# Kernel optimization log

Measured on AMD Instinct MI355X. Metric: run time of the kernel, lower is better.

Reference implementation:

```python
import jax, jax.numpy as jnp
import numpy as np

H, LMAX, NSEG, EPS = 8, 2, 16, 1e-7
S = (LMAX + 1) ** 2  # 9 spherical components
L_OF_M = jnp.asarray(np.floor(np.sqrt(np.arange(S))).astype(np.int32))  # degree l of each m-component


def so3_linear(x, W, b):
    # x [n,S,Cin]; W [LMAX+1,Cin,Cout] per-degree weights; bias only on l=0 (invariant) component
    y = jnp.einsum('nsi,sio->nso', x, W[L_OF_M])
    return y + b[None, None, :] * (jnp.arange(S) == 0)[None, :, None]


def equiv_layernorm(x, gamma, beta):
    # x [N,S,C]; standard LN on l=0 scalars, RMS-of-irrep-norm scaling (equivariant) for l>0
    x0 = x[:, 0, :]
    mu = jnp.mean(x0, -1, keepdims=True)
    var = jnp.mean((x0 - mu) ** 2, -1, keepdims=True)
    outs = [(((x0 - mu) / jnp.sqrt(var + EPS)) * gamma[0] + beta)[:, None, :]]
    for l in range(1, LMAX + 1):
        xl = x[:, l * l:(l + 1) * (l + 1), :]               # [N,2l+1,C]
        n2 = jnp.mean(xl * xl, axis=1)                      # [N,C] mean sq over m
        rms = jnp.sqrt(jnp.mean(n2, -1, keepdims=True) + EPS)  # [N,1]
        outs.append(xl / rms[:, None, :] * gamma[l][None, None, :])
    return jnp.concatenate(outs, axis=1)


def setup_inputs() -> dict:
    key = jax.random.key(0)
    ks = jax.random.split(key, 12)
    N, E, CIN, CH = 512, 8192, 128, 256
    return dict(
        q=jax.random.normal(ks[0], (N, S, CIN), jnp.float32),
        k=jax.random.normal(ks[1], (N, S, CIN), jnp.float32),
        v=jax.random.normal(ks[2], (N, S, CIN), jnp.float32),
        envelope=jax.random.uniform(ks[3], (E,), jnp.float32),
        attn_bias=jax.random.normal(ks[4], (H, E), jnp.float32),
        atom_index=jax.random.randint(ks[5], (E,), 0, N),
        batch_index=jnp.sort(jax.random.randint(ks[6], (E,), 0, NSEG)),
        edge_map_tab=jax.random.randint(ks[7], (E,), 0, E),
        Wq=jax.random.normal(ks[8], (LMAX + 1, CIN, CH), jnp.float32) / np.float32(np.sqrt(CIN)),
        bq=jnp.zeros((CH,), jnp.float32),
        Wk=jax.random.normal(ks[9], (LMAX + 1, CIN, CH), jnp.float32) / np.float32(np.sqrt(CIN)),
        bk=jnp.zeros((CH,), jnp.float32),
        Wv=jax.random.normal(ks[10], (LMAX + 1, CIN, CH), jnp.float32) / np.float32(np.sqrt(CIN)),
        bv=jnp.zeros((CH,), jnp.float32),
        gamma=jnp.ones((LMAX + 1, CH), jnp.float32),
        beta=jnp.zeros((CH,), jnp.float32),
        Wo=jax.random.normal(ks[11], (LMAX + 1, CH, CIN), jnp.float32) / np.float32(np.sqrt(CH)),
        bo=jnp.zeros((CIN,), jnp.float32),
    )


def reference(q, k, v, envelope, attn_bias, atom_index, batch_index, edge_map_tab,
              Wq, bq, Wk, bk, Wv, bv, gamma, beta, Wo, bo):
    N, E = q.shape[0], atom_index.shape[0]
    qh = so3_linear(q, Wq, bq)                      # [N,S,CH]
    kh = so3_linear(k, Wk, bk)[atom_index]          # [E,S,CH] gather per edge
    vh = so3_linear(v, Wv, bv)[atom_index]
    CH = qh.shape[-1]
    d = CH // H
    qh = qh.reshape(N, S, H, d).transpose(2, 0, 1, 3).reshape(H, N, S * d)
    kh = kh.reshape(E, S, H, d).transpose(2, 0, 1, 3).reshape(H, E, S * d)
    vh = vh.reshape(E, S, H, d).transpose(2, 0, 1, 3).reshape(H, E, S * d)
    scale = np.float32(np.sqrt(d / 3.0) / d)
    scores = jnp.einsum('hnf,hef->hne', qh * scale, kh)         # [H,N,E]
    scores = scores + attn_bias[:, edge_map_tab][:, None, :]
    env_e = envelope[edge_map_tab]                               # [E]
    # smooth scatter softmax grouped by batch_index over edge axis
    st = scores.transpose(2, 0, 1)                               # [E,H,N]
    mx = jax.ops.segment_max(st, batch_index, num_segments=NSEG)
    rec = jnp.exp(st - mx[batch_index]) * env_e[:, None, None]
    den = jax.ops.segment_sum(rec, batch_index, num_segments=NSEG)
    attn = rec / (den[batch_index] + 1e-16)
    attn = (attn * env_e[:, None, None]).transpose(1, 2, 0)      # [H,N,E]
    out = jnp.einsum('hne,hef->hnf', attn, vh)                   # [H,N,S*d]
    out = out.transpose(1, 0, 2).reshape(N, H, S, d).transpose(0, 2, 1, 3).reshape(N, S, CH)
    out = equiv_layernorm(out, gamma, beta)
    return so3_linear(out, Wo, bo)
```

## Files before the change

kernel.cpp:

```cpp
#include <hip/hip_runtime.h>
#include <hip/hip_bf16.h>
#include <math.h>

#define NH 8
#define SDIM 9
#define NSEG 16
#define NATOM 512
#define NEDGE 8192
#define CIN 128
#define CHN 256
#define DH 32
#define FDIM 288
#define EPS 1e-7f
#define SCALE 0.10206207261596577f

typedef __attribute__((ext_vector_type(8))) short bf16x8;
typedef __attribute__((ext_vector_type(8))) short short8;
typedef __attribute__((ext_vector_type(4))) float f32x4;

__device__ inline float blockReduceMax(float v, float* red) {
    #pragma unroll
    for (int off = 32; off; off >>= 1) v = fmaxf(v, __shfl_xor(v, off, 64));
    int lane = threadIdx.x & 63, wid = threadIdx.x >> 6;
    if (lane == 0) red[wid] = v;
    __syncthreads();
    v = fmaxf(fmaxf(red[0], red[1]), fmaxf(red[2], red[3]));
    __syncthreads();
    return v;
}
__device__ inline int lower_bound_batch(const int* __restrict__ b, int val) {
    int lo = 0, hi = NEDGE;
    while (lo < hi) {
        int mid = (lo + hi) >> 1;
        if (b[mid] < val) lo = mid + 1; else hi = mid;
    }
    return lo;
}
__device__ inline ushort f2bu(float x) {
    __hip_bfloat16 b = __float2bfloat16(x);
    return *(ushort*)&b;
}

__global__ void __launch_bounds__(256) wtrans(const float* __restrict__ Wq, const float* __restrict__ Wk,
                                              const float* __restrict__ Wv, const float* __restrict__ Wo,
                                              ushort* __restrict__ WqT, ushort* __restrict__ WkT,
                                              ushort* __restrict__ WvT, ushort* __restrict__ WoT) {
    const int bid = blockIdx.x;
    const int tid = threadIdx.x;
    __shared__ float tile[64][33];
    const float* src; ushort* dst; int R, C, r0, c0;
    if (bid < 144) {
        const int z = bid / 48;
        const int rem = bid % 48;
        const int l = rem >> 4;
        const int t = rem & 15;
        R = CIN; C = CHN;
        r0 = (t >> 3) * 64; c0 = (t & 7) * 32;
        src = ((z == 0) ? Wq : (z == 1) ? Wk : Wv) + (size_t)l * R * C;
        dst = ((z == 0) ? WqT : (z == 1) ? WkT : WvT) + (size_t)l * R * C;
    } else {
        const int rem = bid - 144;
        const int l = rem >> 4;
        const int t = rem & 15;
        R = CHN; C = CIN;
        r0 = (t >> 2) * 64; c0 = (t & 3) * 32;
        src = Wo + (size_t)l * R * C;
        dst = WoT + (size_t)l * R * C;
    }
    #pragma unroll
    for (int p = 0; p < 8; ++p) {
        int row = p * 8 + (tid >> 5);
        int col = tid & 31;
        tile[row][col] = src[(size_t)(r0 + row) * C + c0 + col];
    }
    __syncthreads();
    #pragma unroll
    for (int p = 0; p < 8; ++p) {
        int c = p * 4 + (tid >> 6);
        int rr = tid & 63;
        dst[(size_t)(c0 + c) * R + r0 + rr] = f2bu(tile[rr][c]);
    }
}

__global__ void __launch_bounds__(256) stage1(const int* __restrict__ batch,
                                              const int* __restrict__ am, const int* __restrict__ emap,
                                              const float* __restrict__ envelope,
                                              const float* __restrict__ attn_bias,
                                              float* __restrict__ E1, float* __restrict__ E2,
                                              const float* __restrict__ q, const float* __restrict__ k,
                                              const float* __restrict__ v,
                                              const ushort* __restrict__ WqT, const ushort* __restrict__ WkT,
                                              const ushort* __restrict__ WvT,
                                              const float* __restrict__ bq, const float* __restrict__ bk,
                                              const float* __restrict__ bv,
                                              ushort* __restrict__ qhB,
                                              ushort* __restrict__ khB,
                                              ushort* __restrict__ vhT,
                                              float* __restrict__ stats) {
    const int bid = blockIdx.x;
    const int tid = threadIdx.x;
    if (bid < NSEG * NH) {
        const int seg = bid & (NSEG - 1), h = bid >> 4;
        __shared__ float e1[NATOM];
        __shared__ float e2[NATOM];
        __shared__ float red[4];
        e1[tid] = 0.f; e1[tid + 256] = 0.f;
        e2[tid] = 0.f; e2[tid + 256] = 0.f;
        const float* bh = attn_bias + (size_t)h * NEDGE;
        float mv = -1e30f;
        for (int e = tid; e < NEDGE; e += 256) mv = fmaxf(mv, bh[e]);
        const float mb = blockReduceMax(mv, red);
        const int st = lower_bound_batch(batch, seg);
        const int en = lower_bound_batch(batch, seg + 1);
        for (int e = st + tid; e < en; e += 256) {
            int m = am[e], em = emap[e];
            float ev = envelope[em];
            float eb = __expf(bh[em] - mb);
            atomicAdd(&e1[m], ev * eb);
            atomicAdd(&e2[m], ev * ev * eb);
        }
        __syncthreads();
        size_t base = ((size_t)h * NSEG + seg) * NATOM;
        E1[base + tid] = e1[tid]; E1[base + tid + 256] = e1[tid + 256];
        E2[base + tid] = e2[tid]; E2[base + tid + 256] = e2[tid + 256];
        return;
    }
    if (bid < NSEG * NH + 432) {
        const int idx = bid - NSEG * NH;
        const int z = idx / 144;
        const int rem = idx - z * 144;
        const int s = rem >> 4;
        const int n0 = (rem & 15) * 32;
        const int l = (s == 0) ? 0 : ((s < 4) ? 1 : 2);
        const float* x = (z == 0) ? q : (z == 1) ? k : v;
        const ushort* WT = ((z == 0) ? WqT : (z == 1) ? WkT : WvT) + (size_t)l * CIN * CHN;
        const float* bias = (z == 0) ? bq : (z == 1) ? bk : bv;
        const int lane = tid & 63, w = tid >> 6;
        const int wr = w >> 1, wc = w & 1;
        const int r = lane & 15, kg = lane >> 4;
        const int arow = n0 + 16 * wr + r;
        const float* xrow = x + ((size_t)arow * SDIM + s) * CIN;
        f32x4 acc[8] = {};
        #pragma unroll
        for (int ks = 0; ks < 4; ++ks) {
            const int k0 = ks * 32 + kg * 8;
            float4 x0 = *(const float4*)(xrow + k0);
            float4 x1 = *(const float4*)(xrow + k0 + 4);
            bf16x8 a;
            a[0] = f2bu(x0.x); a[1] = f2bu(x0.y); a[2] = f2bu(x0.z); a[3] = f2bu(x0.w);
            a[4] = f2bu(x1.x); a[5] = f2bu(x1.y); a[6] = f2bu(x1.z); a[7] = f2bu(x1.w);
            #pragma unroll
            for (int j = 0; j < 8; ++j) {
                const int o = 128 * wc + 16 * j + r;
                bf16x8 bf = *(const bf16x8*)(WT + (size_t)o * CIN + k0);
                acc[j] = __builtin_amdgcn_mfma_f32_16x16x32_bf16(a, bf, acc[j], 0, 0, 0);
            }
        }
        const float sc = (z == 0) ? SCALE : 1.0f;
        #pragma unroll
        for (int j = 0; j < 8; ++j) {
            const int o = 128 * wc + 16 * j + r;
            const float bb = (s == 0) ? bias[o] : 0.f;
            const int h = o >> 5, dj = o & 31;
            const int f = s * DH + dj;
            if (z < 2) {
                ushort* dst = (z == 0) ? qhB : khB;
                #pragma unroll
                for (int p = 0; p < 4; ++p) {
                    int row = n0 + 16 * wr + kg * 4 + p;
                    dst[((size_t)h * NATOM + row) * FDIM + f] = f2bu((acc[j][p] + bb) * sc);
                }
            } else {
                ushort* dst = vhT + ((size_t)h * FDIM + f) * NATOM;
                #pragma unroll
                for (int p = 0; p < 4; ++p) {
                    int row = n0 + 16 * wr + kg * 4 + p;
                    dst[row] = f2bu(acc[j][p] + bb);
                }
            }
        }
        return;
    }
    {
        float4 z4 = {0.f, 0.f, 0.f, 0.f};
        float4* sp = (float4*)stats;
        sp[tid] = z4;
        sp[tid + 256] = z4;
    }
}

#define SBST 520
__global__ void __launch_bounds__(512) attn_fused(const ushort* __restrict__ qhB,
                                                  const ushort* __restrict__ khB,
                                                  const float* __restrict__ E1,
                                                  const float* __restrict__ E2,
                                                  ushort* __restrict__ attnB) {
    const int h = blockIdx.y;
    const int n0 = blockIdx.x * 16;
    __shared__ ushort sbuf[16 * SBST];
    __shared__ float rowmax[8][16];
    __shared__ float Dpart[8][16][NSEG];
    __shared__ float invDs[16][NSEG];
    const int tid = threadIdx.x;
    const int lane = tid & 63, w = tid >> 6;
    const int r = lane & 15, kg = lane >> 4;
    const ushort* A = qhB + (size_t)h * NATOM * FDIM;
    const ushort* B = khB + (size_t)h * NATOM * FDIM;
    const float* e1g = E1 + (size_t)h * NSEG * NATOM;
    const float* e2g = E2 + (size_t)h * NSEG * NATOM;
    const int ar = n0 + r;
    f32x4 acc[4] = {};
    #pragma unroll
    for (int ks = 0; ks < FDIM / 32; ++ks) {
        const int k0 = ks * 32 + kg * 8;
        bf16x8 a = *(const bf16x8*)(A + (size_t)ar * FDIM + k0);
        #pragma unroll
        for (int j = 0; j < 4; ++j) {
            const int bcol = w * 64 + 16 * j + r;
            bf16x8 b = *(const bf16x8*)(B + (size_t)bcol * FDIM + k0);
            acc[j] = __builtin_amdgcn_mfma_f32_16x16x32_bf16(a, b, acc[j], 0, 0, 0);
        }
    }
    float pm[4];
    #pragma unroll
    for (int p = 0; p < 4; ++p) {
        float m = fmaxf(fmaxf(acc[0][p], acc[1][p]), fmaxf(acc[2][p], acc[3][p]));
        pm[p] = m;
    }
    #pragma unroll
    for (int mk = 1; mk < 16; mk <<= 1)
        #pragma unroll
        for (int p = 0; p < 4; ++p) pm[p] = fmaxf(pm[p], __shfl_xor(pm[p], mk, 64));
    if (r == 0) {
        #pragma unroll
        for (int p = 0; p < 4; ++p) rowmax[w][kg * 4 + p] = pm[p];
    }
    __syncthreads();
    float mx[4];
    #pragma unroll
    for (int p = 0; p < 4; ++p) {
        const int row = kg * 4 + p;
        float m = rowmax[0][row];
        #pragma unroll
        for (int ww2 = 1; ww2 < 8; ++ww2) m = fmaxf(m, rowmax[ww2][row]);
        mx[p] = m;
    }
    float es[4][4];
    #pragma unroll
    for (int j = 0; j < 4; ++j)
        #pragma unroll
        for (int p = 0; p < 4; ++p) es[j][p] = __expf(acc[j][p] - mx[p]);
    float Dp[4][NSEG] = {};
    #pragma unroll
    for (int j = 0; j < 4; ++j) {
        const int col = w * 64 + 16 * j + r;
        #pragma unroll
        for (int g = 0; g < NSEG; ++g) {
            float e1 = e1g[(size_t)g * NATOM + col];
            #pragma unroll
            for (int p = 0; p < 4; ++p) Dp[p][g] += es[j][p] * e1;
        }
    }
    #pragma unroll
    for (int mk = 1; mk < 16; mk <<= 1)
        #pragma unroll
        for (int p = 0; p < 4; ++p)
            #pragma unroll
            for (int g = 0; g < NSEG; ++g) Dp[p][g] += __shfl_xor(Dp[p][g], mk, 64);
    if (r == 0) {
        #pragma unroll
        for (int p = 0; p < 4; ++p)
            #pragma unroll
            for (int g = 0; g < NSEG; ++g) Dpart[w][kg * 4 + p][g] = Dp[p][g];
    }
    __syncthreads();
    if (tid < 256) {
        const int row = tid >> 4, g = tid & 15;
        float d = 0.f;
        #pragma unroll
        for (int ww2 = 0; ww2 < 8; ++ww2) d += Dpart[ww2][row][g];
        invDs[row][g] = 1.0f / (d + 1e-30f);
    }
    __syncthreads();
    float iv[4][NSEG];
    #pragma unroll
    for (int p = 0; p < 4; ++p)
        #pragma unroll
        for (int g = 0; g < NSEG; ++g) iv[p][g] = invDs[kg * 4 + p][g];
    #pragma unroll
    for (int j = 0; j < 4; ++j) {
        const int col = w * 64 + 16 * j + r;
        float ww[4] = {};
        #pragma unroll
        for (int g = 0; g < NSEG; ++g) {
            float e2 = e2g[(size_t)g * NATOM + col];
            #pragma unroll
            for (int p = 0; p < 4; ++p) ww[p] += e2 * iv[p][g];
        }
        #pragma unroll
        for (int p = 0; p < 4; ++p)
            sbuf[(kg * 4 + p) * SBST + col] = f2bu(es[j][p] * ww[p]);
    }
    __syncthreads();
    {
        ushort* dst = attnB + ((size_t)h * NATOM + n0) * NATOM;
        #pragma unroll
        for (int i = tid * 8; i < 16 * NATOM; i += 4096) {
            const int row = i >> 9, col = i & 511;
            *(short8*)(dst + (size_t)row * NATOM + col) = *(short8*)(sbuf + row * SBST + col);
        }
    }
}

__global__ void __launch_bounds__(256) gemm_out_stats(const ushort* __restrict__ attnB,
                                                      const ushort* __restrict__ vhT,
                                                      float* __restrict__ attnOut,
                                                      float* __restrict__ stats) {
    const int h = blockIdx.z;
    const int fb = blockIdx.x;
    const int n0 = blockIdx.y * 64;
    const int tid = threadIdx.x;
    const int lane = tid & 63, w = tid >> 6;
    const int r = lane & 15, kg = lane >> 4;
    const ushort* A = attnB + (size_t)h * NATOM * NATOM;
    const ushort* B = vhT + (size_t)h * FDIM * NATOM;
    const int ar = n0 + 16 * w + r;
    f32x4 acc[2] = {};
    #pragma unroll 4
    for (int ks = 0; ks < NATOM / 32; ++ks) {
        const int k0 = ks * 32 + kg * 8;
        bf16x8 a = *(const bf16x8*)(A + (size_t)ar * NATOM + k0);
        bf16x8 b0 = *(const bf16x8*)(B + (size_t)(32 * fb + r) * NATOM + k0);
        bf16x8 b1 = *(const bf16x8*)(B + (size_t)(32 * fb + 16 + r) * NATOM + k0);
        acc[0] = __builtin_amdgcn_mfma_f32_16x16x32_bf16(a, b0, acc[0], 0, 0, 0);
        acc[1] = __builtin_amdgcn_mfma_f32_16x16x32_bf16(a, b1, acc[1], 0, 0, 0);
    }
    float sA[4], sB[4];
    #pragma unroll
    for (int p = 0; p < 4; ++p) { sA[p] = 0.f; sB[p] = 0.f; }
    #pragma unroll
    for (int j = 0; j < 2; ++j) {
        const int dj = 16 * j + r;
        #pragma unroll
        for (int p = 0; p < 4; ++p) {
            const int row = n0 + 16 * w + kg * 4 + p;
            float x = acc[j][p];
            attnOut[((size_t)row * SDIM + fb) * CHN + h * DH + dj] = x;
            sA[p] += x;
            sB[p] += x * x;
        }
    }
    #pragma unroll
    for (int mk = 1; mk < 16; mk <<= 1)
        #pragma unroll
        for (int p = 0; p < 4; ++p) {
            sA[p] += __shfl_xor(sA[p], mk, 64);
            sB[p] += __shfl_xor(sB[p], mk, 64);
        }
    if (r == 0) {
        #pragma unroll
        for (int p = 0; p < 4; ++p) {
            const int row = n0 + 16 * w + kg * 4 + p;
            if (fb == 0) {
                atomicAdd(&stats[row * 4 + 0], sA[p]);
                atomicAdd(&stats[row * 4 + 1], sB[p]);
            } else if (fb < 4) {
                atomicAdd(&stats[row * 4 + 2], sB[p]);
            } else {
                atomicAdd(&stats[row * 4 + 3], sB[p]);
            }
        }
    }
}

__global__ void __launch_bounds__(256) so3out_ln(const float* __restrict__ attnOut,
                                                 const float* __restrict__ stats,
                                                 const float* __restrict__ gamma,
                                                 const float* __restrict__ beta,
                                                 const ushort* __restrict__ WoT,
                                                 const float* __restrict__ bo,
                                                 float* __restrict__ out) {
    const int s = blockIdx.y;
    const int n0 = blockIdx.x * 16;
    const int l = (s == 0) ? 0 : ((s < 4) ? 1 : 2);
    const int tid = threadIdx.x;
    const int lane = tid & 63, w = tid >> 6;
    const int r = lane & 15, kg = lane >> 4;
    const int ar = n0 + r;
    float mu, ivl;
    {
        float s0 = stats[ar * 4 + 0];
        float q0 = stats[ar * 4 + 1];
        float q1 = stats[ar * 4 + 2];
        float q2 = stats[ar * 4 + 3];
        float m0 = s0 * (1.0f / CHN);
        float var = q0 * (1.0f / CHN) - m0 * m0;
        if (s == 0) { mu = m0; ivl = 1.0f / sqrtf(var + EPS); }
        else if (s < 4) { mu = 0.f; ivl = 1.0f / sqrtf(q1 * (1.0f / (3 * CHN)) + EPS); }
        else { mu = 0.f; ivl = 1.0f / sqrtf(q2 * (1.0f / (5 * CHN)) + EPS); }
    }
    const float* xrow = attnOut + ((size_t)ar * SDIM + s) * CHN;
    const float* gl = gamma + l * CHN;
    const ushort* B = WoT + (size_t)l * CIN * CHN;
    f32x4 acc[2] = {};
    #pragma unroll
    for (int ks = 0; ks < CHN / 32; ++ks) {
        const int k0 = ks * 32 + kg * 8;
        float4 x0 = *(const float4*)(xrow + k0);
        float4 x1 = *(const float4*)(xrow + k0 + 4);
        float4 g0 = *(const float4*)(gl + k0);
        float4 g1 = *(const float4*)(gl + k0 + 4);
        float y[8];
        y[0] = (x0.x - mu) * ivl * g0.x; y[1] = (x0.y - mu) * ivl * g0.y;
        y[2] = (x0.z - mu) * ivl * g0.z; y[3] = (x0.w - mu) * ivl * g0.w;
        y[4] = (x1.x - mu) * ivl * g1.x; y[5] = (x1.y - mu) * ivl * g1.y;
        y[6] = (x1.z - mu) * ivl * g1.z; y[7] = (x1.w - mu) * ivl * g1.w;
        if (s == 0) {
            float4 b0 = *(const float4*)(beta + k0);
            float4 b1 = *(const float4*)(beta + k0 + 4);
            y[0] += b0.x; y[1] += b0.y; y[2] += b0.z; y[3] += b0.w;
            y[4] += b1.x; y[5] += b1.y; y[6] += b1.z; y[7] += b1.w;
        }
        bf16x8 a;
        #pragma unroll
        for (int jj = 0; jj < 8; ++jj) a[jj] = f2bu(y[jj]);
        bf16x8 b0f = *(const bf16x8*)(B + (size_t)(32 * w + r) * CHN + k0);
        bf16x8 b1f = *(const bf16x8*)(B + (size_t)(32 * w + 16 + r) * CHN + k0);
        acc[0] = __builtin_amdgcn_mfma_f32_16x16x32_bf16(a, b0f, acc[0], 0, 0, 0);
        acc[1] = __builtin_amdgcn_mfma_f32_16x16x32_bf16(a, b1f, acc[1], 0, 0, 0);
    }
    #pragma unroll
    for (int j = 0; j < 2; ++j) {
        const int o = 32 * w + 16 * j + r;
        const float badd = (s == 0) ? bo[o] : 0.f;
        #pragma unroll
        for (int p = 0; p < 4; ++p) {
            const int n = n0 + kg * 4 + p;
            out[((size_t)n * SDIM + s) * CIN + o] = acc[j][p] + badd;
        }
    }
}

extern "C" void kernel_launch(void* const* d_in, const int* in_sizes, int n_in,
                              void* d_out, int out_size, void* d_ws, size_t ws_size,
                              hipStream_t stream) {
    const float* q = (const float*)d_in[0];
    const float* k = (const float*)d_in[1];
    const float* v = (const float*)d_in[2];
    const float* envelope = (const float*)d_in[3];
    const float* attn_bias = (const float*)d_in[4];
    const int* atom_index = (const int*)d_in[5];
    const int* batch_index = (const int*)d_in[6];
    const int* edge_map = (const int*)d_in[7];
    const float* Wq = (const float*)d_in[8];
    const float* bq = (const float*)d_in[9];
    const float* Wk = (const float*)d_in[10];
    const float* bk = (const float*)d_in[11];
    const float* Wv = (const float*)d_in[12];
    const float* bv = (const float*)d_in[13];
    const float* gamma = (const float*)d_in[14];
    const float* beta = (const float*)d_in[15];
    const float* Wo = (const float*)d_in[16];
    const float* bo = (const float*)d_in[17];
    float* out = (float*)d_out;

    const size_t SZ_HNF = (size_t)NH * NATOM * FDIM;
    const size_t SZ_HNN = (size_t)NH * NATOM * NATOM;
    const size_t SZ_TAB = (size_t)NH * NSEG * NATOM;
    const size_t SZ_WOT = (size_t)3 * CIN * CHN;
    const size_t SZ_NSC = (size_t)NATOM * SDIM * CHN;

    char* wsb = (char*)d_ws;
    ushort* qhB = (ushort*)wsb;
    ushort* khB = qhB + SZ_HNF;
    ushort* vhT = khB + SZ_HNF;
    ushort* attnB = vhT + SZ_HNF;
    float* attnOut = (float*)(attnB + SZ_HNN);
    float* E1 = attnOut + SZ_NSC;
    float* E2 = E1 + SZ_TAB;
    ushort* WqT = (ushort*)(E2 + SZ_TAB);
    ushort* WkT = WqT + SZ_WOT;
    ushort* WvT = WkT + SZ_WOT;
    ushort* WoT = WvT + SZ_WOT;
    float* stats = (float*)(WoT + SZ_WOT);

    size_t needed = 2 * 3 * SZ_HNF + 2 * SZ_HNN + 4 * SZ_NSC + 4 * 2 * SZ_TAB
                  + 2 * 4 * SZ_WOT + 4 * NATOM * 4 + 256;
    if (ws_size < needed) return;

    wtrans<<<192, 256, 0, stream>>>(Wq, Wk, Wv, Wo, WqT, WkT, WvT, WoT);
    stage1<<<NSEG * NH + 432 + 1, 256, 0, stream>>>(
        batch_index, atom_index, edge_map, envelope, attn_bias, E1, E2,
        q, k, v, WqT, WkT, WvT, bq, bk, bv, qhB, khB, vhT, stats);
    attn_fused<<<dim3(NATOM / 16, NH), 512, 0, stream>>>(qhB, khB, E1, E2, attnB);
    gemm_out_stats<<<dim3(SDIM, NATOM / 64, NH), 256, 0, stream>>>(attnB, vhT, attnOut, stats);
    so3out_ln<<<dim3(NATOM / 16, SDIM), 256, 0, stream>>>(attnOut, stats, gamma, beta, WoT, bo, out);
}
```

Measured before the change: 79.92 us.

## Drop weight-transpose kernel, read fp32 weights directly, store attention output as bf16

Removes the separate wtrans launch. The Wq/Wk/Wv projections now gather fp32 weights with strided loads and convert them to bf16 inside the MFMA loop, and the Wo transpose moves into extra blocks of stage1. The intermediate attention output is stored as bf16 instead of fp32, which halves its write and read traffic at some cost in precision. The 2D/3D grids of attn_fused and gemm_out_stats are flattened so the head index varies fastest. The strided uncoalesced weight loads in stage1 add memory cost in exchange for saving a kernel launch.

```diff
diff --git a/kernel.cpp b/kernel.cpp
--- a/kernel.cpp
+++ b/kernel.cpp
@@ -40,46 +40,9 @@
     __hip_bfloat16 b = __float2bfloat16(x);
     return *(ushort*)&b;
 }
-
-__global__ void __launch_bounds__(256) wtrans(const float* __restrict__ Wq, const float* __restrict__ Wk,
-                                              const float* __restrict__ Wv, const float* __restrict__ Wo,
-                                              ushort* __restrict__ WqT, ushort* __restrict__ WkT,
-                                              ushort* __restrict__ WvT, ushort* __restrict__ WoT) {
-    const int bid = blockIdx.x;
-    const int tid = threadIdx.x;
-    __shared__ float tile[64][33];
-    const float* src; ushort* dst; int R, C, r0, c0;
-    if (bid < 144) {
-        const int z = bid / 48;
-        const int rem = bid % 48;
-        const int l = rem >> 4;
-        const int t = rem & 15;
-        R = CIN; C = CHN;
-        r0 = (t >> 3) * 64; c0 = (t & 7) * 32;
-        src = ((z == 0) ? Wq : (z == 1) ? Wk : Wv) + (size_t)l * R * C;
-        dst = ((z == 0) ? WqT : (z == 1) ? WkT : WvT) + (size_t)l * R * C;
-    } else {
-        const int rem = bid - 144;
-        const int l = rem >> 4;
-        const int t = rem & 15;
-        R = CHN; C = CIN;
-        r0 = (t >> 2) * 64; c0 = (t & 3) * 32;
-        src = Wo + (size_t)l * R * C;
-        dst = WoT + (size_t)l * R * C;
-    }
-    #pragma unroll
-    for (int p = 0; p < 8; ++p) {
-        int row = p * 8 + (tid >> 5);
-        int col = tid & 31;
-        tile[row][col] = src[(size_t)(r0 + row) * C + c0 + col];
-    }
-    __syncthreads();
-    #pragma unroll
-    for (int p = 0; p < 8; ++p) {
-        int c = p * 4 + (tid >> 6);
-        int rr = tid & 63;
-        dst[(size_t)(c0 + c) * R + r0 + rr] = f2bu(tile[rr][c]);
-    }
+__device__ inline float bu2f(ushort u) {
+    unsigned int v = ((unsigned int)u) << 16;
+    return *(float*)&v;
 }
 
 __global__ void __launch_bounds__(256) stage1(const int* __restrict__ batch,
@@ -89,13 +52,15 @@
                                               float* __restrict__ E1, float* __restrict__ E2,
                                               const float* __restrict__ q, const float* __restrict__ k,
                                               const float* __restrict__ v,
-                                              const ushort* __restrict__ WqT, const ushort* __restrict__ WkT,
-                                              const ushort* __restrict__ WvT,
+                                              const float* __restrict__ Wq, const float* __restrict__ Wk,
+                                              const float* __restrict__ Wv,
                                               const float* __restrict__ bq, const float* __restrict__ bk,
                                               const float* __restrict__ bv,
                                               ushort* __restrict__ qhB,
                                               ushort* __restrict__ khB,
                                               ushort* __restrict__ vhT,
+                                              const float* __restrict__ Wo,
+                                              ushort* __restrict__ WoT,
                                               float* __restrict__ stats) {
     const int bid = blockIdx.x;
     const int tid = threadIdx.x;
@@ -125,15 +90,38 @@
         E2[base + tid] = e2[tid]; E2[base + tid + 256] = e2[tid + 256];
         return;
     }
-    if (bid < NSEG * NH + 432) {
-        const int idx = bid - NSEG * NH;
+    if (bid < NSEG * NH + 48) {
+        const int t = bid - NSEG * NH;
+        const int l = t / 16;
+        const int cb = (t & 15) >> 2, ob = t & 3;
+        const int c0 = cb * 64, o0 = ob * 32;
+        __shared__ float tile[64][33];
+        const float* src = Wo + (size_t)l * CHN * CIN;
+        #pragma unroll
+        for (int p = 0; p < 8; ++p) {
+            int row = p * 8 + (tid >> 5);
+            int col = tid & 31;
+            tile[row][col] = src[(size_t)(c0 + row) * CIN + o0 + col];
+        }
+        __syncthreads();
+        ushort* dst = WoT + (size_t)l * CIN * CHN;
+        #pragma unroll
+        for (int p = 0; p < 8; ++p) {
+            int o = p * 4 + (tid >> 6);
+            int c = tid & 63;
+            dst[(size_t)(o0 + o) * CHN + c0 + c] = f2bu(tile[c][o]);
+        }
+        return;
+    }
+    if (bid < NSEG * NH + 48 + 432) {
+        const int idx = bid - (NSEG * NH + 48);
         const int z = idx / 144;
         const int rem = idx - z * 144;
         const int s = rem >> 4;
         const int n0 = (rem & 15) * 32;
         const int l = (s == 0) ? 0 : ((s < 4) ? 1 : 2);
         const float* x = (z == 0) ? q : (z == 1) ? k : v;
-        const ushort* WT = ((z == 0) ? WqT : (z == 1) ? WkT : WvT) + (size_t)l * CIN * CHN;
+        const float* W = ((z == 0) ? Wq : (z == 1) ? Wk : Wv) + (size_t)l * CIN * CHN;
         const float* bias = (z == 0) ? bq : (z == 1) ? bk : bv;
         const int lane = tid & 63, w = tid >> 6;
         const int wr = w >> 1, wc = w & 1;
@@ -152,7 +140,10 @@
             #pragma unroll
             for (int j = 0; j < 8; ++j) {
                 const int o = 128 * wc + 16 * j + r;
-                bf16x8 bf = *(const bf16x8*)(WT + (size_t)o * CIN + k0);
+                const float* wp = W + (size_t)k0 * CHN + o;
+                bf16x8 bf;
+                #pragma unroll
+                for (int jj = 0; jj < 8; ++jj) bf[jj] = f2bu(wp[(size_t)jj * CHN]);
                 acc[j] = __builtin_amdgcn_mfma_f32_16x16x32_bf16(a, bf, acc[j], 0, 0, 0);
             }
         }
@@ -195,8 +186,8 @@
                                                   const float* __restrict__ E1,
                                                   const float* __restrict__ E2,
                                                   ushort* __restrict__ attnB) {
-    const int h = blockIdx.y;
-    const int n0 = blockIdx.x * 16;
+    const int h = blockIdx.x & 7;
+    const int n0 = (blockIdx.x >> 3) * 16;
     __shared__ ushort sbuf[16 * SBST];
     __shared__ float rowmax[8][16];
     __shared__ float Dpart[8][16][NSEG];
@@ -223,10 +214,8 @@
     }
     float pm[4];
     #pragma unroll
-    for (int p = 0; p < 4; ++p) {
-        float m = fmaxf(fmaxf(acc[0][p], acc[1][p]), fmaxf(acc[2][p], acc[3][p]));
-        pm[p] = m;
-    }
+    for (int p = 0; p < 4; ++p)
+        pm[p] = fmaxf(fmaxf(acc[0][p], acc[1][p]), fmaxf(acc[2][p], acc[3][p]));
     #pragma unroll
     for (int mk = 1; mk < 16; mk <<= 1)
         #pragma unroll
@@ -314,11 +303,12 @@
 
 __global__ void __launch_bounds__(256) gemm_out_stats(const ushort* __restrict__ attnB,
                                                       const ushort* __restrict__ vhT,
-                                                      float* __restrict__ attnOut,
+                                                      ushort* __restrict__ attnOutB,
                                                       float* __restrict__ stats) {
-    const int h = blockIdx.z;
-    const int fb = blockIdx.x;
-    const int n0 = blockIdx.y * 64;
+    const int h = blockIdx.x & 7;
+    const int rest = blockIdx.x >> 3;
+    const int fb = rest % 9;
+    const int n0 = (rest / 9) * 64;
     const int tid = threadIdx.x;
     const int lane = tid & 63, w = tid >> 6;
     const int r = lane & 15, kg = lane >> 4;
@@ -345,7 +335,7 @@
         for (int p = 0; p < 4; ++p) {
             const int row = n0 + 16 * w + kg * 4 + p;
             float x = acc[j][p];
-            attnOut[((size_t)row * SDIM + fb) * CHN + h * DH + dj] = x;
+            attnOutB[((size_t)row * SDIM + fb) * CHN + h * DH + dj] = f2bu(x);
             sA[p] += x;
             sB[p] += x * x;
         }
@@ -373,7 +363,7 @@
     }
 }
 
-__global__ void __launch_bounds__(256) so3out_ln(const float* __restrict__ attnOut,
+__global__ void __launch_bounds__(256) so3out_ln(const ushort* __restrict__ attnOutB,
                                                  const float* __restrict__ stats,
                                                  const float* __restrict__ gamma,
                                                  const float* __restrict__ beta,
@@ -399,22 +389,25 @@
         else if (s < 4) { mu = 0.f; ivl = 1.0f / sqrtf(q1 * (1.0f / (3 * CHN)) + EPS); }
         else { mu = 0.f; ivl = 1.0f / sqrtf(q2 * (1.0f / (5 * CHN)) + EPS); }
     }
-    const float* xrow = attnOut + ((size_t)ar * SDIM + s) * CHN;
+    const ushort* xrow = attnOutB + ((size_t)ar * SDIM + s) * CHN;
     const float* gl = gamma + l * CHN;
     const ushort* B = WoT + (size_t)l * CIN * CHN;
     f32x4 acc[2] = {};
     #pragma unroll
     for (int ks = 0; ks < CHN / 32; ++ks) {
         const int k0 = ks * 32 + kg * 8;
-        float4 x0 = *(const float4*)(xrow + k0);
-        float4 x1 = *(const float4*)(xrow + k0 + 4);
+        bf16x8 x8 = *(const bf16x8*)(xrow + k0);
         float4 g0 = *(const float4*)(gl + k0);
         float4 g1 = *(const float4*)(gl + k0 + 4);
         float y[8];
-        y[0] = (x0.x - mu) * ivl * g0.x; y[1] = (x0.y - mu) * ivl * g0.y;
-        y[2] = (x0.z - mu) * ivl * g0.z; y[3] = (x0.w - mu) * ivl * g0.w;
-        y[4] = (x1.x - mu) * ivl * g1.x; y[5] = (x1.y - mu) * ivl * g1.y;
-        y[6] = (x1.z - mu) * ivl * g1.z; y[7] = (x1.w - mu) * ivl * g1.w;
+        y[0] = (bu2f((ushort)x8[0]) - mu) * ivl * g0.x;
+        y[1] = (bu2f((ushort)x8[1]) - mu) * ivl * g0.y;
+        y[2] = (bu2f((ushort)x8[2]) - mu) * ivl * g0.z;
+        y[3] = (bu2f((ushort)x8[3]) - mu) * ivl * g0.w;
+        y[4] = (bu2f((ushort)x8[4]) - mu) * ivl * g1.x;
+        y[5] = (bu2f((ushort)x8[5]) - mu) * ivl * g1.y;
+        y[6] = (bu2f((ushort)x8[6]) - mu) * ivl * g1.z;
+        y[7] = (bu2f((ushort)x8[7]) - mu) * ivl * g1.w;
         if (s == 0) {
             float4 b0 = *(const float4*)(beta + k0);
             float4 b1 = *(const float4*)(beta + k0 + 4);
@@ -475,24 +468,21 @@
     ushort* khB = qhB + SZ_HNF;
     ushort* vhT = khB + SZ_HNF;
     ushort* attnB = vhT + SZ_HNF;
-    float* attnOut = (float*)(attnB + SZ_HNN);
-    float* E1 = attnOut + SZ_NSC;
+    ushort* attnOutB = attnB + SZ_HNN;
+    float* E1 = (float*)(attnOutB + SZ_NSC);
     float* E2 = E1 + SZ_TAB;
-    ushort* WqT = (ushort*)(E2 + SZ_TAB);
-    ushort* WkT = WqT + SZ_WOT;
-    ushort* WvT = WkT + SZ_WOT;
-    ushort* WoT = WvT + SZ_WOT;
+    ushort* WoT = (ushort*)(E2 + SZ_TAB);
     float* stats = (float*)(WoT + SZ_WOT);
 
-    size_t needed = 2 * 3 * SZ_HNF + 2 * SZ_HNN + 4 * SZ_NSC + 4 * 2 * SZ_TAB
-                  + 2 * 4 * SZ_WOT + 4 * NATOM * 4 + 256;
+    size_t needed = 2 * (3 * SZ_HNF + SZ_HNN + SZ_NSC + SZ_WOT)
+                  + 4 * 2 * SZ_TAB + 4 * NATOM * 4 + 256;
     if (ws_size < needed) return;
 
-    wtrans<<<192, 256, 0, stream>>>(Wq, Wk, Wv, Wo, WqT, WkT, WvT, WoT);
-    stage1<<<NSEG * NH + 432 + 1, 256, 0, stream>>>(
+    stage1<<<NSEG * NH + 48 + 432 + 1, 256, 0, stream>>>(
         batch_index, atom_index, edge_map, envelope, attn_bias, E1, E2,
-        q, k, v, WqT, WkT, WvT, bq, bk, bv, qhB, khB, vhT, stats);
-    attn_fused<<<dim3(NATOM / 16, NH), 512, 0, stream>>>(qhB, khB, E1, E2, attnB);
-    gemm_out_stats<<<dim3(SDIM, NATOM / 64, NH), 256, 0, stream>>>(attnB, vhT, attnOut, stats);
-    so3out_ln<<<dim3(NATOM / 16, SDIM), 256, 0, stream>>>(attnOut, stats, gamma, beta, WoT, bo, out);
-}
+        q, k, v, Wq, Wk, Wv, bq, bk, bv, qhB, khB, vhT, Wo, WoT, stats);
+    attn_fused<<<NATOM / 16 * NH, 512, 0, stream>>>(qhB, khB, E1, E2, attnB);
+    gemm_out_stats<<<SDIM * (NATOM / 64) * NH, 256, 0, stream>>>(attnB, vhT, attnOutB, stats);
+    so3out_ln<<<dim3(NATOM / 16, SDIM), 256, 0, stream>>>(
+        attnOutB, stats, gamma, beta, WoT, bo, out);
+}
```

Measured after the change: 72.75 us, median of 3. -9.0%, faster.
